# Kernel tuning notes

Measured on AMD Instinct MI355X. Metric: run time of the kernel, lower is better.

## Reference

```python
import jax, jax.numpy as jnp
import numpy as np

K = 5
INPLANES = 256
PLANES = 384
M = 4
CM = INPLANES // M  # 64 channels after reduction; also the group count
STRIDE = 1


def setup_inputs() -> dict:
    key = jax.random.key(0)
    ks = jax.random.split(key, 19)

    def w(k, shape, s=0.05):
        return jax.random.normal(k, shape, dtype=jnp.float32) * s

    return {
        "x": jax.random.normal(ks[0], (32, INPLANES, 64, 64), dtype=jnp.float32),
        "conv_w": w(ks[1], (CM, INPLANES)),       # self.conv (1x1)
        "conv_b": w(ks[2], (CM,)),
        "ck_w": w(ks[3], ()),                      # self.conv_k (1->1 1x1 == scalar affine)
        "ck_b": w(ks[4], ()),
        "ck2_w": w(ks[5], ()),                     # self.conv_k2
        "ck2_b": w(ks[6], ()),
        "ckd4_w": w(ks[7], ()),                    # self.conv_k_d4
        "ckd4_b": w(ks[8], ()),
        "kern_w": w(ks[9], (K * K,)),              # self.conv_kernel (1 -> k*k, 1x1)
        "kern_b": w(ks[10], (K * K,)),
        "kern2_w": w(ks[11], (9,)),                # self.conv_kernel2 (1 -> 9)
        "kern2_b": w(ks[12], (9,)),
        "kernd4_w": w(ks[13], (9,)),               # self.conv_kernel_d4 (1 -> 9)
        "kernd4_b": w(ks[14], (9,)),
        "fuse_w": w(ks[15], (PLANES // 3, CM)),    # self.fuse (1x1)
        "fuse_b": w(ks[16], (PLANES // 3,)),
        "fc_w": w(ks[17], (PLANES, PLANES // 3 * 3)),  # self.fuse_channel (1x1)
        "fc_b": w(ks[18], (PLANES,)),
    }


def _depthwise(f, ker, pad, dil):
    # Per-sample depthwise conv: fold batch into channels -> one grouped conv.
    # f: [N, CM, H, W], ker: [N, CM, kh, kw]
    N, Cm, H, W = f.shape
    kh, kw = ker.shape[2], ker.shape[3]
    x = f.reshape(1, N * Cm, H, W)
    wgt = ker.reshape(N * Cm, 1, kh, kw)
    out = jax.lax.conv_general_dilated(
        x, wgt, window_strides=(STRIDE, STRIDE),
        padding=[(pad, pad), (pad, pad)], rhs_dilation=(dil, dil),
        feature_group_count=N * Cm,
        dimension_numbers=('NCHW', 'OIHW', 'NCHW'))
    return out.reshape(N, Cm, out.shape[2], out.shape[3])


def reference(x, conv_w, conv_b, ck_w, ck_b, ck2_w, ck2_b, ckd4_w, ckd4_b,
              kern_w, kern_b, kern2_w, kern2_b, kernd4_w, kernd4_b,
              fuse_w, fuse_b, fc_w, fc_b):
    N = x.shape[0]
    # f = relu(conv(x)), g = relu(conv(avg_pool(x)))
    f = jax.nn.relu(jnp.einsum('nchw,oc->nohw', x, conv_w) + conv_b[None, :, None, None])
    g = jax.nn.relu(jnp.mean(x, axis=(2, 3)) @ conv_w.T + conv_b)  # [N, CM]

    def dyn_kernel(kw, kb, sw, sb, kk):
        # conv_kernel*: scalar g[n,c] -> kk*kk values; conv_k*: scalar affine on top.
        ker = sw * (g[:, :, None] * kw[None, None, :] + kb[None, None, :]) + sb
        return ker.reshape(N, CM, kk, kk)

    k1 = dyn_kernel(kern_w, kern_b, ck_w, ck_b, K)
    k2 = dyn_kernel(kern2_w, kern2_b, ck2_w, ck2_b, 3)
    k3 = dyn_kernel(kernd4_w, kernd4_b, ckd4_w, ckd4_b, 3)

    pad0 = (K - 1) // 2
    o1 = _depthwise(f, k1, pad0, 1)   # k x k, dilation 1
    o2 = _depthwise(f, k2, 2, 2)      # 3x3, dilation 2, pad 2
    o3 = _depthwise(f, k3, 4, 4)      # 3x3, dilation 4, pad 4

    def fuse(o):
        return jnp.einsum('nchw,oc->nohw', o, fuse_w) + fuse_b[None, :, None, None]

    y = jnp.concatenate([fuse(o1), fuse(o2), fuse(o3)], axis=1)
    return jnp.einsum('nchw,oc->nohw', y, fc_w) + fc_b[None, :, None, None]
```

## Files before the change

kernel.cpp:

```cpp
#include <hip/hip_runtime.h>

#define NB   32
#define CIN  256
#define CM   64
#define HWSZ 4096
#define OC   384
#define KTOT 192

typedef __attribute__((ext_vector_type(8))) short bf16x8;
typedef __attribute__((ext_vector_type(4))) float f32x4;

static __device__ __forceinline__ unsigned short f2bf(float v) {
    union { float f; unsigned u; } a; a.f = v;
    unsigned r = a.u + 0x7fffu + ((a.u >> 16) & 1u);
    return (unsigned short)(r >> 16);
}
static __device__ __forceinline__ float bf2f(unsigned short u) {
    union { unsigned u; float f; } a; a.u = ((unsigned)u) << 16;
    return a.f;
}

__global__ void kw_pre(const float* __restrict__ fuse_w, const float* __restrict__ fuse_b,
                       const float* __restrict__ fc_w, const float* __restrict__ fc_b,
                       const float* __restrict__ conv_w,
                       unsigned short* __restrict__ Wb, float* __restrict__ bt,
                       unsigned short* __restrict__ cwb, float* __restrict__ xm) {
    int k = blockIdx.x;
    int o = threadIdx.x;
    if (k == KTOT) {
        __shared__ float fb[128];
        if (o < 128) fb[o] = fuse_b[o];
        __syncthreads();
        float s = fc_b[o];
        #pragma unroll 4
        for (int q = 0; q < 384; ++q) s += fc_w[o * 384 + q] * fb[q & 127];
        bt[o] = s;
        for (int idx = o; idx < CM * CIN; idx += 384) cwb[idx] = f2bf(conv_w[idx]);
        for (int idx = o; idx < NB * CIN; idx += 384) xm[idx] = 0.f;
        return;
    }
    int i = k >> 6, c = k & 63;
    __shared__ float fw[128];
    if (o < 128) fw[o] = fuse_w[o * 64 + c];
    __syncthreads();
    float s = 0.f;
    #pragma unroll 8
    for (int j = 0; j < 128; ++j) s += fc_w[o * 384 + i * 128 + j] * fw[j];
    Wb[o * KTOT + k] = f2bf(s);
}

__global__ void __launch_bounds__(256) k3_fconv(const float* __restrict__ x,
                                                const unsigned short* __restrict__ cwb,
                                                const float* __restrict__ conv_b,
                                                unsigned short* __restrict__ f_t,
                                                float* __restrict__ xm) {
    __shared__ unsigned short Ab[256 * 40];
    __shared__ unsigned short Bb[64 * 264];
    __shared__ float sm[CIN];
    int orig = blockIdx.y * 16 + blockIdx.x;
    int swz = (orig & 7) * 64 + (orig >> 3);
    int pt = swz & 15, n = swz >> 4;
    int p0 = pt * 256;
    int t = threadIdx.x;
    int lane = t & 63;
    int wv = t >> 6;
    int q = lane >> 4, m16 = lane & 15;

    sm[t] = 0.f;

    #pragma unroll
    for (int i = 0; i < 8; ++i) {
        int id = t + i * 256;
        int row = id >> 5, seg = id & 31;
        bf16x8 v = *(const bf16x8*)(cwb + row * CIN + seg * 8);
        *(bf16x8*)(&Bb[row * 264 + seg * 8]) = v;
    }

    f32x4 acc[4][4];
    #pragma unroll
    for (int mt = 0; mt < 4; ++mt)
        #pragma unroll
        for (int nt = 0; nt < 4; ++nt)
            #pragma unroll
            for (int r = 0; r < 4; ++r) acc[mt][nt][r] = 0.f;

    const float* xn = x + (size_t)n * CIN * HWSZ;

    for (int kc = 0; kc < 8; ++kc) {
        __syncthreads();
        #pragma unroll
        for (int i = 0; i < 2; ++i) {
            int id = t + i * 256;
            int kq = id & 7, pg = id >> 3;
            int cin0 = kc * 32 + kq * 4;
            const float* xp = xn + (size_t)cin0 * HWSZ + p0 + pg * 4;
            f32x4 r0 = __builtin_nontemporal_load((const f32x4*)(xp));
            f32x4 r1 = __builtin_nontemporal_load((const f32x4*)(xp + HWSZ));
            f32x4 r2 = __builtin_nontemporal_load((const f32x4*)(xp + 2 * HWSZ));
            f32x4 r3 = __builtin_nontemporal_load((const f32x4*)(xp + 3 * HWSZ));
            uint2 w;
            w.x = (unsigned)f2bf(r0.x) | ((unsigned)f2bf(r1.x) << 16);
            w.y = (unsigned)f2bf(r2.x) | ((unsigned)f2bf(r3.x) << 16);
            *(uint2*)(&Ab[(pg * 4 + 0) * 40 + kq * 4]) = w;
            w.x = (unsigned)f2bf(r0.y) | ((unsigned)f2bf(r1.y) << 16);
            w.y = (unsigned)f2bf(r2.y) | ((unsigned)f2bf(r3.y) << 16);
            *(uint2*)(&Ab[(pg * 4 + 1) * 40 + kq * 4]) = w;
            w.x = (unsigned)f2bf(r0.z) | ((unsigned)f2bf(r1.z) << 16);
            w.y = (unsigned)f2bf(r2.z) | ((unsigned)f2bf(r3.z) << 16);
            *(uint2*)(&Ab[(pg * 4 + 2) * 40 + kq * 4]) = w;
            w.x = (unsigned)f2bf(r0.w) | ((unsigned)f2bf(r1.w) << 16);
            w.y = (unsigned)f2bf(r2.w) | ((unsigned)f2bf(r3.w) << 16);
            *(uint2*)(&Ab[(pg * 4 + 3) * 40 + kq * 4]) = w;
            float s0 = r0.x + r0.y + r0.z + r0.w;
            float s1 = r1.x + r1.y + r1.z + r1.w;
            float s2 = r2.x + r2.y + r2.z + r2.w;
            float s3 = r3.x + r3.y + r3.z + r3.w;
            #pragma unroll
            for (int off = 8; off < 64; off <<= 1) {
                s0 += __shfl_xor(s0, off);
                s1 += __shfl_xor(s1, off);
                s2 += __shfl_xor(s2, off);
                s3 += __shfl_xor(s3, off);
            }
            if (lane < 8) {
                float* sp = &sm[kc * 32 + lane * 4];
                atomicAdd(sp + 0, s0);
                atomicAdd(sp + 1, s1);
                atomicAdd(sp + 2, s2);
                atomicAdd(sp + 3, s3);
            }
        }
        __syncthreads();
        bf16x8 af[4], bfr[4];
        #pragma unroll
        for (int mt = 0; mt < 4; ++mt)
            af[mt] = *(const bf16x8*)(&Ab[(wv * 64 + mt * 16 + m16) * 40 + q * 8]);
        #pragma unroll
        for (int nt = 0; nt < 4; ++nt)
            bfr[nt] = *(const bf16x8*)(&Bb[(nt * 16 + m16) * 264 + kc * 32 + q * 8]);
        #pragma unroll
        for (int mt = 0; mt < 4; ++mt)
            #pragma unroll
            for (int nt = 0; nt < 4; ++nt)
                acc[mt][nt] = __builtin_amdgcn_mfma_f32_16x16x32_bf16(af[mt], bfr[nt], acc[mt][nt], 0, 0, 0);
    }

    atomicAdd(xm + n * CIN + t, sm[t]);

    unsigned short* fo = f_t + (size_t)n * HWSZ * CM;
    #pragma unroll
    for (int nt = 0; nt < 4; ++nt) {
        int ch = nt * 16 + m16;
        float b = conv_b[ch];
        #pragma unroll
        for (int mt = 0; mt < 4; ++mt) {
            int pixb = p0 + wv * 64 + mt * 16 + q * 4;
            #pragma unroll
            for (int r = 0; r < 4; ++r) {
                float v = fmaxf(acc[mt][nt][r] + b, 0.f);
                fo[(size_t)(pixb + r) * CM + ch] = f2bf(v);
            }
        }
    }
}

__global__ void __launch_bounds__(512, 2) k45_dwgemm(const unsigned short* __restrict__ f_t,
                                                     const float* __restrict__ xm,
                                                     const float* __restrict__ conv_w,
                                                     const float* __restrict__ conv_b,
                                                     const float* ck_w, const float* ck_b,
                                                     const float* ck2_w, const float* ck2_b,
                                                     const float* ckd4_w, const float* ckd4_b,
                                                     const float* kern_w, const float* kern_b,
                                                     const float* kern2_w, const float* kern2_b,
                                                     const float* kernd4_w, const float* kernd4_b,
                                                     const unsigned short* __restrict__ Wb,
                                                     const float* __restrict__ bt,
                                                     float* __restrict__ out) {
    __shared__ unsigned short fl[480 * 72];
    __shared__ unsigned short ot[128 * 200];
    __shared__ float bts[128];
    __shared__ float g_sm[CM];
    int orig = blockIdx.y * 32 + blockIdx.x;
    int swz = (orig & 7) * 128 + (orig >> 3);
    int tile = swz & 31, n = swz >> 5;
    int r0 = (tile >> 1) * 4, c0 = (tile & 1) * 32;
    int t = threadIdx.x;
    int lane = t & 63, wv = t >> 6;

    const unsigned short* fn = f_t + (size_t)n * HWSZ * CM;
    #pragma unroll
    for (int i = 0; i < 8; ++i) {
        int id = t + i * 512;
        if (id < 3840) {
            int cg = id & 7, pl = id >> 3;
            int lr = pl / 40, lc = pl - lr * 40;
            int gr = r0 + lr - 4, gc = c0 + lc - 4;
            bf16x8 v;
            if ((unsigned)gr < 64u && (unsigned)gc < 64u) {
                v = *(const bf16x8*)(fn + (size_t)(gr * 64 + gc) * CM + cg * 8);
            } else {
                #pragma unroll
                for (int j = 0; j < 8; ++j) v[j] = 0;
            }
            *(bf16x8*)(&fl[pl * 72 + cg * 8]) = v;
        }
    }
    if (t < CM) {
        const f32x4* xr = (const f32x4*)(xm + (size_t)n * CIN);
        const f32x4* wr = (const f32x4*)(conv_w + t * CIN);
        float a = 0.f;
        #pragma unroll 8
        for (int i = 0; i < CIN / 4; ++i) {
            f32x4 xv = xr[i], wvv = wr[i];
            a = fmaf(xv.x, wvv.x, a); a = fmaf(xv.y, wvv.y, a);
            a = fmaf(xv.z, wvv.z, a); a = fmaf(xv.w, wvv.w, a);
        }
        g_sm[t] = fmaxf(conv_b[t] + a * (1.0f / 4096.0f), 0.f);
    }
    __syncthreads();

    int cp = t & 31;
    int pg = t >> 5;
    float ge = g_sm[cp * 2], go = g_sm[cp * 2 + 1];
    float2 t1[25], t2[9], t3[9];
    {
        float sw = ck_w[0], sb = ck_b[0];
        #pragma unroll
        for (int i = 0; i < 25; ++i) {
            float kw = kern_w[i], kb = kern_b[i];
            t1[i].x = sw * (ge * kw + kb) + sb;
            t1[i].y = sw * (go * kw + kb) + sb;
        }
        sw = ck2_w[0]; sb = ck2_b[0];
        #pragma unroll
        for (int i = 0; i < 9; ++i) {
            float kw = kern2_w[i], kb = kern2_b[i];
            t2[i].x = sw * (ge * kw + kb) + sb;
            t2[i].y = sw * (go * kw + kb) + sb;
        }
        sw = ckd4_w[0]; sb = ckd4_b[0];
        #pragma unroll
        for (int i = 0; i < 9; ++i) {
            float kw = kernd4_w[i], kb = kernd4_b[i];
            t3[i].x = sw * (ge * kw + kb) + sb;
            t3[i].y = sw * (go * kw + kb) + sb;
        }
    }

    for (int pass = 0; pass < 8; ++pass) {
        int pli = pg + pass * 16;
        int row = pli >> 5, col = pli & 31;
        int base = ((row + 4) * 40 + (col + 4)) * 72 + cp * 2;
        float s1e = 0.f, s1o = 0.f, s2e = 0.f, s2o = 0.f, s3e = 0.f, s3o = 0.f;
        #pragma unroll
        for (int ky = 0; ky < 5; ++ky)
            #pragma unroll
            for (int kx = 0; kx < 5; ++kx) {
                unsigned fv = *(const unsigned*)(&fl[base + ((ky - 2) * 40 + (kx - 2)) * 72]);
                float fe = bf2f((unsigned short)(fv & 0xffffu));
                float fo = bf2f((unsigned short)(fv >> 16));
                float2 tp = t1[ky * 5 + kx];
                s1e = fmaf(tp.x, fe, s1e);
                s1o = fmaf(tp.y, fo, s1o);
                if (((ky & 1) | (kx & 1)) == 0) {
                    float2 tq = t2[(ky >> 1) * 3 + (kx >> 1)];
                    s2e = fmaf(tq.x, fe, s2e);
                    s2o = fmaf(tq.y, fo, s2o);
                }
                if (ky == 2 && kx == 2) {
                    float2 tq = t3[4];
                    s3e = fmaf(tq.x, fe, s3e);
                    s3o = fmaf(tq.y, fo, s3o);
                }
            }
        #pragma unroll
        for (int ky = 0; ky < 3; ++ky)
            #pragma unroll
            for (int kx = 0; kx < 3; ++kx) {
                if (ky == 1 && kx == 1) continue;
                unsigned fv = *(const unsigned*)(&fl[base + ((ky * 4 - 4) * 40 + (kx * 4 - 4)) * 72]);
                float2 tp = t3[ky * 3 + kx];
                s3e = fmaf(tp.x, bf2f((unsigned short)(fv & 0xffffu)), s3e);
                s3o = fmaf(tp.y, bf2f((unsigned short)(fv >> 16)), s3o);
            }
        unsigned short* ob = &ot[pli * 200];
        *(unsigned*)(ob + cp * 2)       = (unsigned)f2bf(s1e) | ((unsigned)f2bf(s1o) << 16);
        *(unsigned*)(ob + 64 + cp * 2)  = (unsigned)f2bf(s2e) | ((unsigned)f2bf(s2o) << 16);
        *(unsigned*)(ob + 128 + cp * 2) = (unsigned)f2bf(s3e) | ((unsigned)f2bf(s3o) << 16);
    }

    unsigned short* wbs = fl;
    int wrow = t >> 2, wqk = t & 3;
    int wm = wv & 3, wn = wv >> 2;
    int q = lane >> 4, m16 = lane & 15;
    float* outn0 = out + (size_t)n * OC * HWSZ;
    for (int ocg = 0; ocg < 3; ++ocg) {
        __syncthreads();
        if (t < 128) bts[t] = bt[ocg * 128 + t];
        #pragma unroll
        for (int j = 0; j < 6; ++j) {
            bf16x8 v = *(const bf16x8*)(Wb + (size_t)(ocg * 128 + wrow) * KTOT + wqk * 48 + j * 8);
            *(bf16x8*)(&wbs[wrow * 200 + wqk * 48 + j * 8]) = v;
        }
        __syncthreads();
        f32x4 acc[2][4];
        #pragma unroll
        for (int mt = 0; mt < 2; ++mt)
            #pragma unroll
            for (int nt = 0; nt < 4; ++nt)
                #pragma unroll
                for (int r = 0; r < 4; ++r) acc[mt][nt][r] = 0.f;
        #pragma unroll
        for (int ks = 0; ks < 6; ++ks) {
            bf16x8 af[2], bfr[4];
            #pragma unroll
            for (int mt = 0; mt < 2; ++mt)
                af[mt] = *(const bf16x8*)(&wbs[(wm * 32 + mt * 16 + m16) * 200 + ks * 32 + q * 8]);
            #pragma unroll
            for (int nt = 0; nt < 4; ++nt)
                bfr[nt] = *(const bf16x8*)(&ot[(wn * 64 + nt * 16 + m16) * 200 + ks * 32 + q * 8]);
            #pragma unroll
            for (int mt = 0; mt < 2; ++mt)
                #pragma unroll
                for (int nt = 0; nt < 4; ++nt)
                    acc[mt][nt] = __builtin_amdgcn_mfma_f32_16x16x32_bf16(af[mt], bfr[nt], acc[mt][nt], 0, 0, 0);
        }
        float* outn = outn0 + (size_t)(ocg * 128) * HWSZ;
        #pragma unroll
        for (int mt = 0; mt < 2; ++mt) {
            #pragma unroll
            for (int r = 0; r < 4; ++r) {
                int ocl = wm * 32 + mt * 16 + q * 4 + r;
                float b = bts[ocl];
                #pragma unroll
                for (int nt = 0; nt < 4; ++nt) {
                    int pl = wn * 64 + nt * 16 + m16;
                    int pr = pl >> 5, pc = pl & 31;
                    __builtin_nontemporal_store(acc[mt][nt][r] + b,
                        &outn[(size_t)ocl * HWSZ + (r0 + pr) * 64 + c0 + pc]);
                }
            }
        }
    }
}

extern "C" void kernel_launch(void* const* d_in, const int* in_sizes, int n_in,
                              void* d_out, int out_size, void* d_ws, size_t ws_size,
                              hipStream_t stream) {
    const float* x       = (const float*)d_in[0];
    const float* conv_w  = (const float*)d_in[1];
    const float* conv_b  = (const float*)d_in[2];
    const float* ck_w    = (const float*)d_in[3];
    const float* ck_b    = (const float*)d_in[4];
    const float* ck2_w   = (const float*)d_in[5];
    const float* ck2_b   = (const float*)d_in[6];
    const float* ckd4_w  = (const float*)d_in[7];
    const float* ckd4_b  = (const float*)d_in[8];
    const float* kern_w  = (const float*)d_in[9];
    const float* kern_b  = (const float*)d_in[10];
    const float* kern2_w = (const float*)d_in[11];
    const float* kern2_b = (const float*)d_in[12];
    const float* kernd4_w= (const float*)d_in[13];
    const float* kernd4_b= (const float*)d_in[14];
    const float* fuse_w  = (const float*)d_in[15];
    const float* fuse_b  = (const float*)d_in[16];
    const float* fc_w    = (const float*)d_in[17];
    const float* fc_b    = (const float*)d_in[18];
    float* out = (float*)d_out;

    char* ws = (char*)d_ws;
    float* xm             = (float*)(ws + 0);
    float* bt             = (float*)(ws + 385024);
    unsigned short* Wb    = (unsigned short*)(ws + 386560);
    unsigned short* cwb   = (unsigned short*)(ws + 534016);
    unsigned short* f_t   = (unsigned short*)(ws + 566784);

    kw_pre<<<dim3(193), dim3(384), 0, stream>>>(fuse_w, fuse_b, fc_w, fc_b, conv_w, Wb, bt, cwb, xm);
    k3_fconv<<<dim3(16, NB), dim3(256), 0, stream>>>(x, cwb, conv_b, f_t, xm);
    k45_dwgemm<<<dim3(32, NB), dim3(512), 0, stream>>>(f_t, xm, conv_w, conv_b,
        ck_w, ck_b, ck2_w, ck2_b, ckd4_w, ckd4_b,
        kern_w, kern_b, kern2_w, kern2_b, kernd4_w, kernd4_b, Wb, bt, out);
}
```

Measured before the change: 406.8 us.

## Drop LDS halo tile, read depthwise inputs from global, raise occupancy

Removes the shared-memory halo tile of f and has each thread read its depthwise taps straight from global memory (one channel per thread instead of a bf16 pair). The output GEMM is split into six 64-row channel groups with a smaller weight tile and accumulator set. Launch bounds go from 2 to 4 blocks per SM. This cuts LDS footprint and registers so more blocks can be resident, at the cost of many scalar 2-byte global loads with bounds checks, more passes, and more barriers.

```diff
diff --git a/kernel.cpp b/kernel.cpp
--- a/kernel.cpp
+++ b/kernel.cpp
@@ -164,7 +164,7 @@
     }
 }
 
-__global__ void __launch_bounds__(512, 2) k45_dwgemm(const unsigned short* __restrict__ f_t,
+__global__ void __launch_bounds__(512, 4) k45_dwgemm(const unsigned short* __restrict__ f_t,
                                                      const float* __restrict__ xm,
                                                      const float* __restrict__ conv_w,
                                                      const float* __restrict__ conv_b,
@@ -177,9 +177,9 @@
                                                      const unsigned short* __restrict__ Wb,
                                                      const float* __restrict__ bt,
                                                      float* __restrict__ out) {
-    __shared__ unsigned short fl[480 * 72];
     __shared__ unsigned short ot[128 * 200];
-    __shared__ float bts[128];
+    __shared__ unsigned short wbs[64 * 200];
+    __shared__ float bts[64];
     __shared__ float g_sm[CM];
     int orig = blockIdx.y * 32 + blockIdx.x;
     int swz = (orig & 7) * 128 + (orig >> 3);
@@ -188,24 +188,6 @@
     int t = threadIdx.x;
     int lane = t & 63, wv = t >> 6;
 
-    const unsigned short* fn = f_t + (size_t)n * HWSZ * CM;
-    #pragma unroll
-    for (int i = 0; i < 8; ++i) {
-        int id = t + i * 512;
-        if (id < 3840) {
-            int cg = id & 7, pl = id >> 3;
-            int lr = pl / 40, lc = pl - lr * 40;
-            int gr = r0 + lr - 4, gc = c0 + lc - 4;
-            bf16x8 v;
-            if ((unsigned)gr < 64u && (unsigned)gc < 64u) {
-                v = *(const bf16x8*)(fn + (size_t)(gr * 64 + gc) * CM + cg * 8);
-            } else {
-                #pragma unroll
-                for (int j = 0; j < 8; ++j) v[j] = 0;
-            }
-            *(bf16x8*)(&fl[pl * 72 + cg * 8]) = v;
-        }
-    }
     if (t < CM) {
         const f32x4* xr = (const f32x4*)(xm + (size_t)n * CIN);
         const f32x4* wr = (const f32x4*)(conv_w + t * CIN);
@@ -220,113 +202,94 @@
     }
     __syncthreads();
 
-    int cp = t & 31;
-    int pg = t >> 5;
-    float ge = g_sm[cp * 2], go = g_sm[cp * 2 + 1];
-    float2 t1[25], t2[9], t3[9];
+    int ch = t & 63;
+    int pgw = t >> 6;
+    float gch = g_sm[ch];
+    float t1[25], t2[9], t3[9];
     {
         float sw = ck_w[0], sb = ck_b[0];
         #pragma unroll
-        for (int i = 0; i < 25; ++i) {
-            float kw = kern_w[i], kb = kern_b[i];
-            t1[i].x = sw * (ge * kw + kb) + sb;
-            t1[i].y = sw * (go * kw + kb) + sb;
-        }
+        for (int i = 0; i < 25; ++i) t1[i] = sw * (gch * kern_w[i] + kern_b[i]) + sb;
         sw = ck2_w[0]; sb = ck2_b[0];
         #pragma unroll
-        for (int i = 0; i < 9; ++i) {
-            float kw = kern2_w[i], kb = kern2_b[i];
-            t2[i].x = sw * (ge * kw + kb) + sb;
-            t2[i].y = sw * (go * kw + kb) + sb;
-        }
+        for (int i = 0; i < 9; ++i) t2[i] = sw * (gch * kern2_w[i] + kern2_b[i]) + sb;
         sw = ckd4_w[0]; sb = ckd4_b[0];
         #pragma unroll
-        for (int i = 0; i < 9; ++i) {
-            float kw = kernd4_w[i], kb = kernd4_b[i];
-            t3[i].x = sw * (ge * kw + kb) + sb;
-            t3[i].y = sw * (go * kw + kb) + sb;
-        }
-    }
-
-    for (int pass = 0; pass < 8; ++pass) {
-        int pli = pg + pass * 16;
-        int row = pli >> 5, col = pli & 31;
-        int base = ((row + 4) * 40 + (col + 4)) * 72 + cp * 2;
-        float s1e = 0.f, s1o = 0.f, s2e = 0.f, s2o = 0.f, s3e = 0.f, s3o = 0.f;
+        for (int i = 0; i < 9; ++i) t3[i] = sw * (gch * kernd4_w[i] + kernd4_b[i]) + sb;
+    }
+
+    const unsigned short* fn = f_t + (size_t)n * HWSZ * CM;
+    for (int pass = 0; pass < 16; ++pass) {
+        int pli = pgw + pass * 8;
+        int prb = r0 + (pli >> 5), pcb = c0 + (pli & 31);
+        float s1 = 0.f, s2 = 0.f, s3 = 0.f;
         #pragma unroll
         for (int ky = 0; ky < 5; ++ky)
             #pragma unroll
             for (int kx = 0; kx < 5; ++kx) {
-                unsigned fv = *(const unsigned*)(&fl[base + ((ky - 2) * 40 + (kx - 2)) * 72]);
-                float fe = bf2f((unsigned short)(fv & 0xffffu));
-                float fo = bf2f((unsigned short)(fv >> 16));
-                float2 tp = t1[ky * 5 + kx];
-                s1e = fmaf(tp.x, fe, s1e);
-                s1o = fmaf(tp.y, fo, s1o);
-                if (((ky & 1) | (kx & 1)) == 0) {
-                    float2 tq = t2[(ky >> 1) * 3 + (kx >> 1)];
-                    s2e = fmaf(tq.x, fe, s2e);
-                    s2o = fmaf(tq.y, fo, s2o);
-                }
-                if (ky == 2 && kx == 2) {
-                    float2 tq = t3[4];
-                    s3e = fmaf(tq.x, fe, s3e);
-                    s3o = fmaf(tq.y, fo, s3o);
-                }
+                int pr = prb + ky - 2, pc = pcb + kx - 2;
+                float fe = 0.f;
+                if ((unsigned)pr < 64u && (unsigned)pc < 64u)
+                    fe = bf2f(fn[(size_t)(pr * 64 + pc) * CM + ch]);
+                s1 = fmaf(t1[ky * 5 + kx], fe, s1);
+                if (((ky & 1) | (kx & 1)) == 0)
+                    s2 = fmaf(t2[(ky >> 1) * 3 + (kx >> 1)], fe, s2);
+                if (ky == 2 && kx == 2)
+                    s3 = fmaf(t3[4], fe, s3);
             }
         #pragma unroll
         for (int ky = 0; ky < 3; ++ky)
             #pragma unroll
             for (int kx = 0; kx < 3; ++kx) {
                 if (ky == 1 && kx == 1) continue;
-                unsigned fv = *(const unsigned*)(&fl[base + ((ky * 4 - 4) * 40 + (kx * 4 - 4)) * 72]);
-                float2 tp = t3[ky * 3 + kx];
-                s3e = fmaf(tp.x, bf2f((unsigned short)(fv & 0xffffu)), s3e);
-                s3o = fmaf(tp.y, bf2f((unsigned short)(fv >> 16)), s3o);
+                int pr = prb + ky * 4 - 4, pc = pcb + kx * 4 - 4;
+                float fe = 0.f;
+                if ((unsigned)pr < 64u && (unsigned)pc < 64u)
+                    fe = bf2f(fn[(size_t)(pr * 64 + pc) * CM + ch]);
+                s3 = fmaf(t3[ky * 3 + kx], fe, s3);
             }
         unsigned short* ob = &ot[pli * 200];
-        *(unsigned*)(ob + cp * 2)       = (unsigned)f2bf(s1e) | ((unsigned)f2bf(s1o) << 16);
-        *(unsigned*)(ob + 64 + cp * 2)  = (unsigned)f2bf(s2e) | ((unsigned)f2bf(s2o) << 16);
-        *(unsigned*)(ob + 128 + cp * 2) = (unsigned)f2bf(s3e) | ((unsigned)f2bf(s3o) << 16);
-    }
-
-    unsigned short* wbs = fl;
-    int wrow = t >> 2, wqk = t & 3;
-    int wm = wv & 3, wn = wv >> 2;
+        ob[ch]       = f2bf(s1);
+        ob[64 + ch]  = f2bf(s2);
+        ob[128 + ch] = f2bf(s3);
+    }
+
+    int wrow = t >> 3, wqk = t & 7;
+    int wm = wv & 1, wn = wv >> 1;
     int q = lane >> 4, m16 = lane & 15;
     float* outn0 = out + (size_t)n * OC * HWSZ;
-    for (int ocg = 0; ocg < 3; ++ocg) {
-        __syncthreads();
-        if (t < 128) bts[t] = bt[ocg * 128 + t];
-        #pragma unroll
-        for (int j = 0; j < 6; ++j) {
-            bf16x8 v = *(const bf16x8*)(Wb + (size_t)(ocg * 128 + wrow) * KTOT + wqk * 48 + j * 8);
-            *(bf16x8*)(&wbs[wrow * 200 + wqk * 48 + j * 8]) = v;
-        }
-        __syncthreads();
-        f32x4 acc[2][4];
+    for (int ocg = 0; ocg < 6; ++ocg) {
+        __syncthreads();
+        if (t < 64) bts[t] = bt[ocg * 64 + t];
+        #pragma unroll
+        for (int j = 0; j < 3; ++j) {
+            bf16x8 v = *(const bf16x8*)(Wb + (size_t)(ocg * 64 + wrow) * KTOT + wqk * 24 + j * 8);
+            *(bf16x8*)(&wbs[wrow * 200 + wqk * 24 + j * 8]) = v;
+        }
+        __syncthreads();
+        f32x4 acc[2][2];
         #pragma unroll
         for (int mt = 0; mt < 2; ++mt)
             #pragma unroll
-            for (int nt = 0; nt < 4; ++nt)
+            for (int nt = 0; nt < 2; ++nt)
                 #pragma unroll
                 for (int r = 0; r < 4; ++r) acc[mt][nt][r] = 0.f;
         #pragma unroll
         for (int ks = 0; ks < 6; ++ks) {
-            bf16x8 af[2], bfr[4];
+            bf16x8 af[2], bfr[2];
             #pragma unroll
             for (int mt = 0; mt < 2; ++mt)
                 af[mt] = *(const bf16x8*)(&wbs[(wm * 32 + mt * 16 + m16) * 200 + ks * 32 + q * 8]);
             #pragma unroll
-            for (int nt = 0; nt < 4; ++nt)
-                bfr[nt] = *(const bf16x8*)(&ot[(wn * 64 + nt * 16 + m16) * 200 + ks * 32 + q * 8]);
+            for (int nt = 0; nt < 2; ++nt)
+                bfr[nt] = *(const bf16x8*)(&ot[(wn * 32 + nt * 16 + m16) * 200 + ks * 32 + q * 8]);
             #pragma unroll
             for (int mt = 0; mt < 2; ++mt)
                 #pragma unroll
-                for (int nt = 0; nt < 4; ++nt)
+                for (int nt = 0; nt < 2; ++nt)
                     acc[mt][nt] = __builtin_amdgcn_mfma_f32_16x16x32_bf16(af[mt], bfr[nt], acc[mt][nt], 0, 0, 0);
         }
-        float* outn = outn0 + (size_t)(ocg * 128) * HWSZ;
+        float* outn = outn0 + (size_t)(ocg * 64) * HWSZ;
         #pragma unroll
         for (int mt = 0; mt < 2; ++mt) {
             #pragma unroll
@@ -334,8 +297,8 @@
                 int ocl = wm * 32 + mt * 16 + q * 4 + r;
                 float b = bts[ocl];
                 #pragma unroll
-                for (int nt = 0; nt < 4; ++nt) {
-                    int pl = wn * 64 + nt * 16 + m16;
+                for (int nt = 0; nt < 2; ++nt) {
+                    int pl = wn * 32 + nt * 16 + m16;
                     int pr = pl >> 5, pc = pl & 31;
                     __builtin_nontemporal_store(acc[mt][nt][r] + b,
                         &outn[(size_t)ocl * HWSZ + (r0 + pr) * 64 + c0 + pc]);
```

Result: slower. 507.7 us (+24.8%).
